# Optimization experiments

Measured on AMD Instinct MI355X. Metric: run time of the kernel, lower is better.

Reference implementation:

```python
import jax, jax.numpy as jnp
import numpy as np

N = 100000       # num nodes
E = 1600000      # num edges (avg degree 16)
IN_DIM = 256
EMB_DIM = 128
K = 2            # nlayers: number of propagation steps


def setup_inputs() -> dict:
    key = jax.random.key(0)
    k1, k2, k3, k4, k5 = jax.random.split(key, 5)
    x = jax.random.normal(k1, (N, IN_DIM), dtype=jnp.float32)
    # glorot-initialized linear weight + zero bias
    scale = jnp.sqrt(6.0 / (IN_DIM + EMB_DIM))
    W = jax.random.uniform(k2, (IN_DIM, EMB_DIM), minval=-scale, maxval=scale, dtype=jnp.float32)
    b = jnp.zeros((EMB_DIM,), dtype=jnp.float32)
    edge_src = jax.random.randint(k3, (E,), 0, N, dtype=jnp.int32)
    edge_dst = jax.random.randint(k4, (E,), 0, N, dtype=jnp.int32)
    # normalized-adjacency-like edge weights (positive, ~1/deg scale)
    edge_w = jax.random.uniform(k5, (E,), dtype=jnp.float32) * (1.0 / 16.0)
    return {"x": x, "W": W, "b": b, "edge_src": edge_src, "edge_dst": edge_dst, "edge_w": edge_w}


def reference(x, W, b, edge_src, edge_dst, edge_w):
    # dropout is identity in eval mode; linear + relu
    h = jax.nn.relu(x @ W + b)  # [N, EMB_DIM]
    # k-step sparse propagation: h <- g @ h, g given as COO edge list
    for _ in range(K):
        msg = h[edge_src] * edge_w[:, None]                     # [E, EMB_DIM]
        h = jax.ops.segment_sum(msg, edge_dst, num_segments=N)  # [N, EMB_DIM]
    return h
```

## Files before the change

### kernel.cpp

```cpp
#include <hip/hip_runtime.h>

#define IN_DIM 256
#define EMB 128
#define BKT_SHIFT 9
#define BKT_NODES 512

typedef __attribute__((ext_vector_type(8))) short short8;
typedef __attribute__((ext_vector_type(4))) float f32x4;

__device__ __forceinline__ unsigned short bf16rtne(float f) {
    unsigned int u = __float_as_uint(f);
    return (unsigned short)((u + 0x7fffu + ((u >> 16) & 1u)) >> 16);
}

__device__ __forceinline__ unsigned int packbf2(float lo, float hi) {
    return ((unsigned int)bf16rtne(hi) << 16) | (unsigned int)bf16rtne(lo);
}

__device__ __forceinline__ short8 pack8(float4 f0, float4 f1) {
    union { uint4 u; short8 s; } U;
    asm("v_cvt_pk_bf16_f32 %0, %1, %2" : "=v"(U.u.x) : "v"(f0.x), "v"(f0.y));
    asm("v_cvt_pk_bf16_f32 %0, %1, %2" : "=v"(U.u.y) : "v"(f0.z), "v"(f0.w));
    asm("v_cvt_pk_bf16_f32 %0, %1, %2" : "=v"(U.u.z) : "v"(f1.x), "v"(f1.y));
    asm("v_cvt_pk_bf16_f32 %0, %1, %2" : "=v"(U.u.w) : "v"(f1.z), "v"(f1.w));
    return U.s;
}


__global__ __launch_bounds__(256) void bucket_hist(const int* __restrict__ dst,
                                                   int* __restrict__ ghist, int E) {
    __shared__ int h[256];
    int t = threadIdx.x;
    h[t] = 0;
    __syncthreads();
    int e0 = blockIdx.x * 1024;
    int e1 = min(E, e0 + 1024);
    for (int i = e0 + t; i < e1; i += 256) atomicAdd(&h[dst[i] >> BKT_SHIFT], 1);
    __syncthreads();
    if (h[t]) atomicAdd(&ghist[t], h[t]);
}

__global__ __launch_bounds__(256) void bucket_scan(const int* __restrict__ ghist,
                                                   int* __restrict__ bucket_off,
                                                   int* __restrict__ gcursor,
                                                   int* __restrict__ row_ptr,
                                                   int NB, int N, int E) {
    __shared__ int s[256];
    int t = threadIdx.x;
    int v = (t < NB) ? ghist[t] : 0;
    s[t] = v;
    __syncthreads();
    for (int off = 1; off < 256; off <<= 1) {
        int u = (t >= off) ? s[t - off] : 0;
        __syncthreads();
        s[t] += u;
        __syncthreads();
    }
    int excl = s[t] - v;
    if (t < NB) {
        bucket_off[t] = excl;
        gcursor[t] = excl;
    }
    if (t == 0) {
        bucket_off[NB] = E;
        row_ptr[N] = E;
    }
}


__global__ __launch_bounds__(512) void bin_scatter(const int* __restrict__ src,
                                                   const int* __restrict__ dst,
                                                   const float* __restrict__ w,
                                                   int* __restrict__ gcursor,
                                                   int2* __restrict__ binned, int E) {
    __shared__ int h[256];
    __shared__ int cur[256];
    int t = threadIdx.x;
    if (t < 256) h[t] = 0;
    __syncthreads();
    int e0 = blockIdx.x * 4096;
    int e1 = min(E, e0 + 4096);
    for (int i = e0 + t; i < e1; i += 512) atomicAdd(&h[dst[i] >> BKT_SHIFT], 1);
    __syncthreads();
    if (t < 256) cur[t] = h[t] ? atomicAdd(&gcursor[t], h[t]) : 0;
    __syncthreads();
    for (int i = e0 + t; i < e1; i += 512) {
        int d = dst[i];
        int b = d >> BKT_SHIFT;
        int ld = d & (BKT_NODES - 1);
        int pos = atomicAdd(&cur[b], 1);
        int2 r;
        r.x = src[i] | (ld << 17);
        r.y = __float_as_int(w[i]);
        binned[pos] = r;
    }
}


__global__ __launch_bounds__(1024) void bucket_sort(const int2* __restrict__ binned,
                                                    const int* __restrict__ bucket_off,
                                                    int2* __restrict__ sorted,
                                                    int* __restrict__ row_ptr, int N) {
    __shared__ int cnt[BKT_NODES];
    __shared__ int cur[BKT_NODES];
    __shared__ int scn[BKT_NODES];
    int t = threadIdx.x;
    int b = blockIdx.x;
    int node0 = b << BKT_SHIFT;
    int nn = min(BKT_NODES, N - node0);
    int beg = bucket_off[b];
    int endb = bucket_off[b + 1];
    if (t < BKT_NODES) cnt[t] = 0;
    __syncthreads();
    for (int i = beg + t; i < endb; i += 1024) {
        int ld = ((unsigned int)binned[i].x) >> 17;
        atomicAdd(&cnt[ld], 1);
    }
    __syncthreads();
    int v = 0;
    if (t < BKT_NODES) {
        v = cnt[t];
        scn[t] = v;
    }
    __syncthreads();
    for (int off = 1; off < BKT_NODES; off <<= 1) {
        int u = 0;
        if (t < BKT_NODES && t >= off) u = scn[t - off];
        __syncthreads();
        if (t < BKT_NODES) scn[t] += u;
        __syncthreads();
    }
    if (t < BKT_NODES) {
        int ep = beg + scn[t] - v;
        cur[t] = ep;
        if (t < nn) row_ptr[node0 + t] = ep;
    }
    __syncthreads();
    for (int i = beg + t; i < endb; i += 1024) {
        int2 r = binned[i];
        int ld = ((unsigned int)r.x) >> 17;
        int pos = atomicAdd(&cur[ld], 1);
        r.x &= 0x1FFFF;
        sorted[pos] = r;
    }
}


__global__ __launch_bounds__(256) void wt_cast(const float* __restrict__ W,
                                               unsigned short* __restrict__ wtg) {
    int i = blockIdx.x * 256 + threadIdx.x;
    int c = i & 127;
    int k = i >> 7;
    wtg[c * 256 + k] = bf16rtne(W[(size_t)k * 128 + c]);
}


__global__ __launch_bounds__(256) void x_cast(const float* __restrict__ x,
                                              unsigned short* __restrict__ xb, int total8) {
    int stride = gridDim.x * 256;
    for (int i = blockIdx.x * 256 + threadIdx.x; i < total8; i += stride) {
        const float4* s = (const float4*)(x + (size_t)i * 8);
        *(short8*)(xb + (size_t)i * 8) = pack8(s[0], s[1]);
    }
}


__global__ __launch_bounds__(256) void gemm_mfma(const unsigned short* __restrict__ xb,
                                                 const unsigned short* __restrict__ wtg,
                                                 const float* __restrict__ bias,
                                                 unsigned short* __restrict__ hbf, int N) {
    __shared__ unsigned short As[128][64];
    __shared__ unsigned short Bs[128][64];
    int tid = threadIdx.x;
    int wv = tid >> 6;
    int lane = tid & 63;
    int lr = lane & 15;
    int lg = lane >> 4;
    int wr = wv * 32;
    int row0 = blockIdx.x * 128;

    f32x4 acc[2][8];
#pragma unroll
    for (int m = 0; m < 2; ++m)
#pragma unroll
        for (int n = 0; n < 8; ++n) acc[m][n] = (f32x4){0.f, 0.f, 0.f, 0.f};

    int p0 = wv * 4 * 64 + lane;

    for (int kb = 0; kb < IN_DIM; kb += 64) {
#pragma unroll
        for (int i = 0; i < 4; ++i) {
            int p = p0 + i * 64;
            int r = p >> 3;
            int c = p & 7;
            int cs = (c ^ (r & 7)) * 8;
            int gr = row0 + r;
            if (gr >= N) gr = N - 1;
            const unsigned short* ga = xb + (size_t)gr * IN_DIM + kb + cs;
            __builtin_amdgcn_global_load_lds(
                (const __attribute__((address_space(1))) void*)ga,
                (__attribute__((address_space(3))) void*)((char*)&As[0][0] + (size_t)(wv * 4 + i) * 1024),
                16, 0, 0);
            const unsigned short* gb = wtg + (size_t)r * IN_DIM + kb + cs;
            __builtin_amdgcn_global_load_lds(
                (const __attribute__((address_space(1))) void*)gb,
                (__attribute__((address_space(3))) void*)((char*)&Bs[0][0] + (size_t)(wv * 4 + i) * 1024),
                16, 0, 0);
        }
        __syncthreads();

        short8 a[2][2];
#pragma unroll
        for (int m = 0; m < 2; ++m)
#pragma unroll
            for (int kk = 0; kk < 2; ++kk) {
                int r = wr + m * 16 + lr;
                int ch = kk * 4 + lg;
                a[m][kk] = *(const short8*)&As[r][((ch ^ (r & 7)) * 8)];
            }
#pragma unroll
        for (int n = 0; n < 8; ++n) {
            int cc = n * 16 + lr;
            int sw = cc & 7;
            short8 b0 = *(const short8*)&Bs[cc][(((0 * 4 + lg) ^ sw) * 8)];
            short8 b1 = *(const short8*)&Bs[cc][(((1 * 4 + lg) ^ sw) * 8)];
            acc[0][n] = __builtin_amdgcn_mfma_f32_16x16x32_bf16(a[0][0], b0, acc[0][n], 0, 0, 0);
            acc[0][n] = __builtin_amdgcn_mfma_f32_16x16x32_bf16(a[0][1], b1, acc[0][n], 0, 0, 0);
            acc[1][n] = __builtin_amdgcn_mfma_f32_16x16x32_bf16(a[1][0], b0, acc[1][n], 0, 0, 0);
            acc[1][n] = __builtin_amdgcn_mfma_f32_16x16x32_bf16(a[1][1], b1, acc[1][n], 0, 0, 0);
        }
        __syncthreads();
    }

#pragma unroll
    for (int n = 0; n < 8; ++n) {
        int c = n * 16 + lr;
        float bv = bias[c];
#pragma unroll
        for (int m = 0; m < 2; ++m) {
#pragma unroll
            for (int j = 0; j < 4; ++j) {
                int r = row0 + wr + m * 16 + lg * 4 + j;
                if (r < N) {
                    float v = fmaxf(acc[m][n][j] + bv, 0.f);
                    hbf[(size_t)r * EMB + c] = bf16rtne(v);
                }
            }
        }
    }
}


template <int OUTBF>
__global__ __launch_bounds__(256) void prop_g(const unsigned int* __restrict__ hin,
                                              void* __restrict__ hout,
                                              const int* __restrict__ rp,
                                              const int2* __restrict__ rec, int N) {
    int wvid = threadIdx.x >> 6;
    int lane = threadIdx.x & 63;
    int node = blockIdx.x * 4 + wvid;
    if (node >= N) return;
    int beg = __builtin_amdgcn_readfirstlane(rp[node]);
    int end = __builtin_amdgcn_readfirstlane(rp[node + 1]);
    float ax = 0.f, ay = 0.f;
    for (int c0 = beg; c0 < end; c0 += 64) {
        int cnt = end - c0;
        if (cnt > 64) cnt = 64;
        int li = lane < cnt ? lane : 0;
        int2 r = rec[c0 + li];
        for (int jb = 0; jb < cnt; jb += 8) {
            int ssrc[8];
            float sw[8];
#pragma unroll
            for (int k = 0; k < 8; ++k) {
                int jj = jb + k;
                int jc = jj < cnt ? jj : 0;
                ssrc[k] = __builtin_amdgcn_readlane(r.x, jc);
                float wv = __uint_as_float((unsigned int)__builtin_amdgcn_readlane(r.y, jc));
                sw[k] = (jj < cnt) ? wv : 0.f;
            }
            unsigned int g[8];
#pragma unroll
            for (int k = 0; k < 8; ++k) g[k] = hin[(size_t)ssrc[k] * 64 + lane];
#pragma unroll
            for (int k = 0; k < 8; ++k) {
                ax = fmaf(sw[k], __uint_as_float(g[k] << 16), ax);
                ay = fmaf(sw[k], __uint_as_float(g[k] & 0xffff0000u), ay);
            }
        }
    }
    if (OUTBF) {
        ((unsigned int*)hout)[(size_t)node * 64 + lane] = packbf2(ax, ay);
    } else {
        float2 o;
        o.x = ax;
        o.y = ay;
        ((float2*)hout)[(size_t)node * 64 + lane] = o;
    }
}


extern "C" void kernel_launch(void* const* d_in, const int* in_sizes, int n_in,
                              void* d_out, int out_size, void* d_ws, size_t ws_size,
                              hipStream_t stream) {
    const float* x = (const float*)d_in[0];
    const float* W = (const float*)d_in[1];
    const float* b = (const float*)d_in[2];
    const int* esrc = (const int*)d_in[3];
    const int* edst = (const int*)d_in[4];
    const float* ew = (const float*)d_in[5];
    int N = in_sizes[0] / IN_DIM;
    int E = in_sizes[3];
    int NB = (N + BKT_NODES - 1) >> BKT_SHIFT;

    char* p = (char*)d_ws;
    auto alloc = [&](size_t bytes) -> void* {
        void* r = (void*)p;
        p += (bytes + 255) & ~(size_t)255;
        return r;
    };
    unsigned short* hbf = (unsigned short*)alloc((size_t)N * EMB * 2);
    unsigned short* h1bf = (unsigned short*)alloc((size_t)N * EMB * 2);
    unsigned short* wtg = (unsigned short*)alloc((size_t)IN_DIM * EMB * 2);
    unsigned short* xbf = (unsigned short*)alloc((size_t)N * IN_DIM * 2);
    int* ghist = (int*)alloc(256 * 4);
    int* gcursor = (int*)alloc(256 * 4);
    int* bucket_off = (int*)alloc((size_t)(NB + 1) * 4);
    int* row_ptr = (int*)alloc((size_t)(N + 1) * 4);
    int2* binned = (int2*)alloc((size_t)E * 8);
    int2* sorted = (int2*)alloc((size_t)E * 8);

    hipMemsetAsync(ghist, 0, 256 * 4, stream);
    wt_cast<<<(IN_DIM * EMB) / 256, 256, 0, stream>>>(W, wtg);
    x_cast<<<2048, 256, 0, stream>>>(x, xbf, N * IN_DIM / 8);
    bucket_hist<<<(E + 1023) / 1024, 256, 0, stream>>>(edst, ghist, E);
    bucket_scan<<<1, 256, 0, stream>>>(ghist, bucket_off, gcursor, row_ptr, NB, N, E);
    bin_scatter<<<(E + 4095) / 4096, 512, 0, stream>>>(esrc, edst, ew, gcursor, binned, E);
    bucket_sort<<<NB, 1024, 0, stream>>>(binned, bucket_off, sorted, row_ptr, N);

    gemm_mfma<<<(N + 127) / 128, 256, 0, stream>>>(xbf, wtg, b, hbf, N);
    prop_g<1><<<(N + 3) / 4, 256, 0, stream>>>((const unsigned int*)hbf, h1bf, row_ptr, sorted, N);
    prop_g<0><<<(N + 3) / 4, 256, 0, stream>>>((const unsigned int*)h1bf, d_out, row_ptr, sorted, N);
}
```

Measured before the change: 264.0 us.

## Stage binned and sorted edges in LDS for coalesced global writes

bin_scatter now loads each block's edges into registers once, computes local bucket offsets with a shared-memory scan, and stages records in LDS so the global writes to binned land in contiguous runs. bucket_sort likewise sorts a bucket's edges into an LDS buffer and writes them out sequentially, falling back to direct scattered writes when a bucket exceeds the buffer capacity. The aim is to replace scattered 8-byte global stores with coalesced ones. The cost is large shared-memory use (about 48KB stage in bin_scatter, about 96KB in bucket_sort), which lowers occupancy, plus extra barriers and a scan.

```diff
diff --git a/kernel.cpp b/kernel.cpp
--- a/kernel.cpp
+++ b/kernel.cpp
@@ -4,6 +4,8 @@
 #define EMB 128
 #define BKT_SHIFT 9
 #define BKT_NODES 512
+#define BINE 4096
+#define SCAP 12288
 
 typedef __attribute__((ext_vector_type(8))) short short8;
 typedef __attribute__((ext_vector_type(4))) float f32x4;
@@ -74,25 +76,69 @@
                                                    int* __restrict__ gcursor,
                                                    int2* __restrict__ binned, int E) {
     __shared__ int h[256];
-    __shared__ int cur[256];
+    __shared__ int lbase[256];
+    __shared__ int gbase[256];
+    __shared__ int lcur[256];
+    __shared__ int2 stage[BINE];
+    __shared__ unsigned char sb[BINE];
     int t = threadIdx.x;
+    int e0 = blockIdx.x * BINE;
+    int e1 = min(E, e0 + BINE);
+    int n = e1 - e0;
+
+    int ed[8], es[8];
+    float ewv[8];
+#pragma unroll
+    for (int j = 0; j < 8; ++j) {
+        int i = e0 + t + j * 512;
+        if (i < e1) {
+            ed[j] = dst[i];
+            es[j] = src[i];
+            ewv[j] = w[i];
+        } else
+            ed[j] = -1;
+    }
     if (t < 256) h[t] = 0;
     __syncthreads();
-    int e0 = blockIdx.x * 4096;
-    int e1 = min(E, e0 + 4096);
-    for (int i = e0 + t; i < e1; i += 512) atomicAdd(&h[dst[i] >> BKT_SHIFT], 1);
-    __syncthreads();
-    if (t < 256) cur[t] = h[t] ? atomicAdd(&gcursor[t], h[t]) : 0;
-    __syncthreads();
-    for (int i = e0 + t; i < e1; i += 512) {
-        int d = dst[i];
-        int b = d >> BKT_SHIFT;
-        int ld = d & (BKT_NODES - 1);
-        int pos = atomicAdd(&cur[b], 1);
-        int2 r;
-        r.x = src[i] | (ld << 17);
-        r.y = __float_as_int(w[i]);
-        binned[pos] = r;
+#pragma unroll
+    for (int j = 0; j < 8; ++j)
+        if (ed[j] >= 0) atomicAdd(&h[ed[j] >> BKT_SHIFT], 1);
+    __syncthreads();
+    int v = 0;
+    if (t < 256) {
+        v = h[t];
+        lbase[t] = v;
+    }
+    __syncthreads();
+    for (int off = 1; off < 256; off <<= 1) {
+        int u = 0;
+        if (t < 256 && t >= off) u = lbase[t - off];
+        __syncthreads();
+        if (t < 256) lbase[t] += u;
+        __syncthreads();
+    }
+    if (t < 256) {
+        lbase[t] -= v;
+        lcur[t] = lbase[t];
+        gbase[t] = v ? atomicAdd(&gcursor[t], v) : 0;
+    }
+    __syncthreads();
+#pragma unroll
+    for (int j = 0; j < 8; ++j) {
+        if (ed[j] >= 0) {
+            int b = ed[j] >> BKT_SHIFT;
+            int p = atomicAdd(&lcur[b], 1);
+            int2 r;
+            r.x = es[j] | ((ed[j] & (BKT_NODES - 1)) << 17);
+            r.y = __float_as_int(ewv[j]);
+            stage[p] = r;
+            sb[p] = (unsigned char)b;
+        }
+    }
+    __syncthreads();
+    for (int i = t; i < n; i += 512) {
+        int b = sb[i];
+        binned[gbase[b] + (i - lbase[b])] = stage[i];
     }
 }
 
@@ -104,12 +150,14 @@
     __shared__ int cnt[BKT_NODES];
     __shared__ int cur[BKT_NODES];
     __shared__ int scn[BKT_NODES];
+    __shared__ int2 stage[SCAP];
     int t = threadIdx.x;
     int b = blockIdx.x;
     int node0 = b << BKT_SHIFT;
     int nn = min(BKT_NODES, N - node0);
     int beg = bucket_off[b];
     int endb = bucket_off[b + 1];
+    int n = endb - beg;
     if (t < BKT_NODES) cnt[t] = 0;
     __syncthreads();
     for (int i = beg + t; i < endb; i += 1024) {
@@ -131,17 +179,29 @@
         __syncthreads();
     }
     if (t < BKT_NODES) {
-        int ep = beg + scn[t] - v;
-        cur[t] = ep;
-        if (t < nn) row_ptr[node0 + t] = ep;
-    }
-    __syncthreads();
-    for (int i = beg + t; i < endb; i += 1024) {
-        int2 r = binned[i];
-        int ld = ((unsigned int)r.x) >> 17;
-        int pos = atomicAdd(&cur[ld], 1);
-        r.x &= 0x1FFFF;
-        sorted[pos] = r;
+        int excl = scn[t] - v;
+        cur[t] = excl;
+        if (t < nn) row_ptr[node0 + t] = beg + excl;
+    }
+    __syncthreads();
+    if (n <= SCAP) {
+        for (int i = beg + t; i < endb; i += 1024) {
+            int2 r = binned[i];
+            int ld = ((unsigned int)r.x) >> 17;
+            int p = atomicAdd(&cur[ld], 1);
+            r.x &= 0x1FFFF;
+            stage[p] = r;
+        }
+        __syncthreads();
+        for (int i = t; i < n; i += 1024) sorted[beg + i] = stage[i];
+    } else {
+        for (int i = beg + t; i < endb; i += 1024) {
+            int2 r = binned[i];
+            int ld = ((unsigned int)r.x) >> 17;
+            int p = atomicAdd(&cur[ld], 1);
+            r.x &= 0x1FFFF;
+            sorted[beg + p] = r;
+        }
     }
 }
 
@@ -335,7 +395,7 @@
     x_cast<<<2048, 256, 0, stream>>>(x, xbf, N * IN_DIM / 8);
     bucket_hist<<<(E + 1023) / 1024, 256, 0, stream>>>(edst, ghist, E);
     bucket_scan<<<1, 256, 0, stream>>>(ghist, bucket_off, gcursor, row_ptr, NB, N, E);
-    bin_scatter<<<(E + 4095) / 4096, 512, 0, stream>>>(esrc, edst, ew, gcursor, binned, E);
+    bin_scatter<<<(E + BINE - 1) / BINE, 512, 0, stream>>>(esrc, edst, ew, gcursor, binned, E);
     bucket_sort<<<NB, 1024, 0, stream>>>(binned, bucket_off, sorted, row_ptr, N);
 
     gemm_mfma<<<(N + 127) / 128, 256, 0, stream>>>(xbf, wtg, b, hbf, N);
```

After: 242.7 us. 1.09x faster.
